# Kernel optimization log

Hardware: AMD Instinct MI355X
Metric: run time of the kernel (lower is better)

## Reference

```python
import jax, jax.numpy as jnp
import numpy as np

N = 50000      # nodes
E = 800000     # edges (avg degree 16)
IN = 128       # in_feats
HID = 32       # hidden_feats per head
H = 4          # num_heads
NEG_SLOPE = 0.2


def setup_inputs() -> dict:
    key = jax.random.key(0)
    ks = jax.random.split(key, 13)
    x = jax.random.normal(ks[0], (N, IN), jnp.float32)
    src = jax.random.randint(ks[1], (E,), 0, N, jnp.int32)
    dst = jax.random.randint(ks[2], (E,), 0, N, jnp.int32)

    def lin(k, fi, fo):
        return jax.random.normal(k, (fi, fo), jnp.float32) * (1.0 / np.sqrt(fi))

    # conv1: IN -> H*HID
    W1 = lin(ks[3], IN, H * HID)
    al1 = jax.random.normal(ks[4], (H, HID), jnp.float32) * 0.1
    ar1 = jax.random.normal(ks[5], (H, HID), jnp.float32) * 0.1
    b1 = jnp.zeros((H, HID), jnp.float32)
    # conv2: H*HID -> H*HID
    W2 = lin(ks[6], H * HID, H * HID)
    al2 = jax.random.normal(ks[7], (H, HID), jnp.float32) * 0.1
    ar2 = jax.random.normal(ks[8], (H, HID), jnp.float32) * 0.1
    b2 = jnp.zeros((H, HID), jnp.float32)
    # fc: HID -> 1
    fcW = lin(ks[9], HID, 1)
    fcb = jnp.zeros((1,), jnp.float32)
    return {"x": x, "src": src, "dst": dst,
            "W1": W1, "al1": al1, "ar1": ar1, "b1": b1,
            "W2": W2, "al2": al2, "ar2": ar2, "b2": b2,
            "fcW": fcW, "fcb": fcb}


def gat_conv(x, src, dst, W, al, ar, b):
    # x: [N, F_in] -> feat: [N, H, HID]
    feat = (x @ W).reshape(N, H, HID)
    el = jnp.sum(feat * al, axis=-1)            # [N, H]
    er = jnp.sum(feat * ar, axis=-1)            # [N, H]
    e = jax.nn.leaky_relu(el[src] + er[dst], NEG_SLOPE)  # [E, H]
    # segment softmax over incoming edges of each dst node
    m = jax.ops.segment_max(e, dst, num_segments=N)      # [N, H]
    ex = jnp.exp(e - m[dst])                              # [E, H]
    denom = jax.ops.segment_sum(ex, dst, num_segments=N)  # [N, H]
    alpha = ex / denom[dst]                                # [E, H]
    msg = feat[src] * alpha[:, :, None]                    # [E, H, HID]
    out = jax.ops.segment_sum(msg, dst, num_segments=N)   # [N, H, HID]
    return out + b[None, :, :]


def reference(x, src, dst, W1, al1, ar1, b1, W2, al2, ar2, b2, fcW, fcb):
    h = gat_conv(x, src, dst, W1, al1, ar1, b1).reshape(N, H * HID)
    h = jax.nn.relu(h)
    # dropout(0.5) is identity in eval mode
    h = gat_conv(h, src, dst, W2, al2, ar2, b2).mean(axis=1)  # [N, HID]
    return h @ fcW + fcb                                       # [N, 1]
```

## Files before the change

### kernel.cpp

```cpp
#include <hip/hip_runtime.h>
#include <hip/hip_fp16.h>

#define LEAK 0.2f
#define CAP 64

static __device__ inline unsigned pack_h2(float a, float b) {
    __half2 h = __floats2half2_rn(a, b);
    unsigned u; __builtin_memcpy(&u, &h, 4); return u;
}
static __device__ inline float2 unpack_h2(unsigned u) {
    __half2 h; __builtin_memcpy(&h, &u, 4); return __half22float2(h);
}

__global__ __launch_bounds__(256) void k0(
    int* __restrict__ cnt, const float* __restrict__ W2,
    const float* __restrict__ al2, const float* __restrict__ ar2,
    const float* __restrict__ fcW, const float* __restrict__ b2,
    float* __restrict__ WfT, float* __restrict__ bc, int N, int zb) {
    const int t = threadIdx.x;
    int i = blockIdx.x * 256 + t;
    if (i < N) cnt[i] = 0;
    int fb = blockIdx.x - zb;
    if (fb >= 0) {
        int idx = fb * 256 + t;
        if (idx < 1536) {
            int c = idx >> 7, k = idx & 127;
            int h = c & 3, sel = c >> 2;
            const float* vec = (sel == 0) ? (al2 + 32 * h)
                             : (sel == 1) ? (ar2 + 32 * h) : fcW;
            float s = 0.f;
#pragma unroll 8
            for (int m = 0; m < 32; m++) s += W2[k * 128 + 32 * h + m] * vec[m];
            WfT[c * 128 + k] = s;
        } else if (idx < 1540) {
            int h = idx - 1536;
            float s = 0.f;
            for (int m = 0; m < 32; m++) s += b2[h * 32 + m] * fcW[m];
            bc[h] = s;
        }
    }
}

__global__ __launch_bounds__(256, 4) void k1(
    const float* __restrict__ X, const float* __restrict__ W,
    const float* __restrict__ al, const float* __restrict__ ar,
    float* __restrict__ elh, float* __restrict__ erh,
    uint2* __restrict__ fh2,
    const int* __restrict__ src, const int* __restrict__ dst,
    int* __restrict__ cnt, unsigned short* __restrict__ ell,
    int N, int E, int ntiles, int nranks) {
    __shared__ float sW[32 * 128];
    __shared__ float sXT[32 * 128];
    const int b = blockIdx.x;
    const int t = threadIdx.x;

    if (b < ntiles) {
        const int r0 = b * 128;
        const int tx = t & 15;
        const int ty = t >> 4;
        const float4* X4 = (const float4*)X;
        const float4* W4 = (const float4*)W;
        float4* sW4 = (float4*)sW;
        const float4* sXT4 = (const float4*)sXT;

        float4 acc[8][2];
#pragma unroll
        for (int r = 0; r < 8; r++) {
            acc[r][0] = make_float4(0.f, 0.f, 0.f, 0.f);
            acc[r][1] = make_float4(0.f, 0.f, 0.f, 0.f);
        }
        for (int ks = 0; ks < 4; ++ks) {
            if (ks) __syncthreads();
#pragma unroll
            for (int i = 0; i < 4; i++) {
                int idx = i * 256 + t;
                sW4[idx] = W4[1024 * ks + idx];
            }
#pragma unroll
            for (int i = 0; i < 4; i++) {
                int idx = i * 256 + t;
                int row = idx >> 3;
                int kq = idx & 7;
                float4 v = make_float4(0.f, 0.f, 0.f, 0.f);
                if (r0 + row < N) v = X4[(size_t)(r0 + row) * 32 + ks * 8 + kq];
                int sc = (((row >> 2) ^ kq)) * 4 + (row & 3);
                sXT[(4 * kq + 0) * 128 + sc] = v.x;
                sXT[(4 * kq + 1) * 128 + sc] = v.y;
                sXT[(4 * kq + 2) * 128 + sc] = v.z;
                sXT[(4 * kq + 3) * 128 + sc] = v.w;
            }
            __syncthreads();
#pragma unroll 4
            for (int k = 0; k < 32; k++) {
                float4 w0 = sW4[k * 32 + tx];
                float4 w1 = sW4[k * 32 + 16 + tx];
                float4 x0 = sXT4[k * 32 + (ty ^ (k >> 2))];
                float4 x1 = sXT4[k * 32 + ((16 + ty) ^ (k >> 2))];
                float xs[8] = {x0.x, x0.y, x0.z, x0.w, x1.x, x1.y, x1.z, x1.w};
#pragma unroll
                for (int r = 0; r < 8; r++) {
                    acc[r][0].x += xs[r] * w0.x; acc[r][0].y += xs[r] * w0.y;
                    acc[r][0].z += xs[r] * w0.z; acc[r][0].w += xs[r] * w0.w;
                    acc[r][1].x += xs[r] * w1.x; acc[r][1].y += xs[r] * w1.y;
                    acc[r][1].z += xs[r] * w1.z; acc[r][1].w += xs[r] * w1.w;
                }
            }
        }
        const float4* al4p = (const float4*)al;
        const float4* ar4p = (const float4*)ar;
        float4 alA = al4p[tx], alB = al4p[16 + tx];
        float4 arA = ar4p[tx], arB = ar4p[16 + tx];
        const int hA = tx >> 3;
        const int hB = 2 + (tx >> 3);
        const int pA = tx & 7;
#pragma unroll
        for (int r = 0; r < 8; r++) {
            int lrow = (r < 4) ? (ty * 4 + r) : (64 + ty * 4 + (r - 4));
            int row = r0 + lrow;
            bool ok = row < N;
            float4 a0 = acc[r][0], a1 = acc[r][1];
            if (ok) {
                uint2 d0, d1;
                d0.x = pack_h2(a0.x, a0.y); d0.y = pack_h2(a0.z, a0.w);
                d1.x = pack_h2(a1.x, a1.y); d1.y = pack_h2(a1.z, a1.w);
                fh2[((size_t)hA * N + row) * 8 + pA] = d0;
                fh2[((size_t)hB * N + row) * 8 + pA] = d1;
            }
            float elA = a0.x * alA.x + a0.y * alA.y + a0.z * alA.z + a0.w * alA.w;
            float erA = a0.x * arA.x + a0.y * arA.y + a0.z * arA.z + a0.w * arA.w;
            float elB = a1.x * alB.x + a1.y * alB.y + a1.z * alB.z + a1.w * alB.w;
            float erB = a1.x * arB.x + a1.y * arB.y + a1.z * arB.z + a1.w * arB.w;
#pragma unroll
            for (int off = 1; off < 8; off <<= 1) {
                elA += __shfl_xor(elA, off); erA += __shfl_xor(erA, off);
                elB += __shfl_xor(elB, off); erB += __shfl_xor(erB, off);
            }
            if (ok && tx == 0) {
                elh[(size_t)0 * N + row] = elA; erh[(size_t)0 * N + row] = erA;
                elh[(size_t)2 * N + row] = elB; erh[(size_t)2 * N + row] = erB;
            }
            if (ok && tx == 8) {
                elh[(size_t)1 * N + row] = elA; erh[(size_t)1 * N + row] = erA;
                elh[(size_t)3 * N + row] = elB; erh[(size_t)3 * N + row] = erB;
            }
        }
    } else {
        const int bE = b - ntiles;
        const int part = bE & 7;
        const int rank = bE >> 3;
        const int S = (N + 7) >> 3;
        const int lo = part * S;
        const int hi = (lo + S < N) ? (lo + S) : N;
        const int per = (E + nranks - 1) / nranks;
        const int e0 = rank * per;
        const int e1 = (e0 + per < E) ? (e0 + per) : E;
        for (int e = e0 + t; e < e1; e += 256) {
            int d = dst[e];
            if (d >= lo && d < hi) {
                int s = src[e];
                int pos = atomicAdd(&cnt[d], 1);
                if (pos < CAP) ell[(size_t)d * CAP + pos] = (unsigned short)s;
            }
        }
    }
}

__global__ __launch_bounds__(256) void k_agg1(
    const uint2* __restrict__ fh2, const float* __restrict__ elh,
    const float* __restrict__ erh, const unsigned short* __restrict__ ell,
    const int* __restrict__ cnt, const float* __restrict__ b1,
    uint2* __restrict__ h1h2, int N, int ngrp) {
    const int wave = threadIdx.x >> 6;
    const int lane = threadIdx.x & 63;
    const int b = blockIdx.x;
    const int h = (b & 7) >> 1;
    const int g = (b >> 3) * 2 + (b & 1);
    if (g >= ngrp) return;
    const int nsub = lane >> 3;
    const int p = lane & 7;
    const int n = g * 32 + wave * 8 + nsub;
    const bool nok = n < N;

    int deg = 0;
    float er = 0.f;
    if (nok) {
        deg = cnt[n]; if (deg > CAP) deg = CAP;
        er = erh[(size_t)h * N + n];
    }
    const float* elp = elh + (size_t)h * N;
    const uint2* fhp = fh2 + (size_t)h * N * 8;
    const unsigned short* row = ell + (size_t)(nok ? n : 0) * CAP;

    float a0 = 0.f, a1 = 0.f, a2 = 0.f, a3 = 0.f, den = 0.f;
    int j = 0;
    for (; j + 3 < deg; j += 4) {
        ushort4 ss = *(const ushort4*)(row + j);
        int s0 = ss.x, s1 = ss.y, s2 = ss.z, s3 = ss.w;
        float e0 = elp[s0] + er;
        float e1 = elp[s1] + er;
        float e2 = elp[s2] + er;
        float e3 = elp[s3] + er;
        uint2 u0 = fhp[(size_t)s0 * 8 + p];
        uint2 u1 = fhp[(size_t)s1 * 8 + p];
        uint2 u2 = fhp[(size_t)s2 * 8 + p];
        uint2 u3 = fhp[(size_t)s3 * 8 + p];
        e0 = fmaxf(e0, LEAK * e0); float w0 = __expf(e0);
        e1 = fmaxf(e1, LEAK * e1); float w1 = __expf(e1);
        e2 = fmaxf(e2, LEAK * e2); float w2 = __expf(e2);
        e3 = fmaxf(e3, LEAK * e3); float w3 = __expf(e3);
        float2 f00 = unpack_h2(u0.x), f01 = unpack_h2(u0.y);
        float2 f10 = unpack_h2(u1.x), f11 = unpack_h2(u1.y);
        float2 f20 = unpack_h2(u2.x), f21 = unpack_h2(u2.y);
        float2 f30 = unpack_h2(u3.x), f31 = unpack_h2(u3.y);
        a0 += w0 * f00.x + w1 * f10.x + w2 * f20.x + w3 * f30.x;
        a1 += w0 * f00.y + w1 * f10.y + w2 * f20.y + w3 * f30.y;
        a2 += w0 * f01.x + w1 * f11.x + w2 * f21.x + w3 * f31.x;
        a3 += w0 * f01.y + w1 * f11.y + w2 * f21.y + w3 * f31.y;
        den += (w0 + w1) + (w2 + w3);
    }
    for (; j < deg; ++j) {
        int s = row[j];
        float e = elp[s] + er;
        uint2 u = fhp[(size_t)s * 8 + p];
        e = fmaxf(e, LEAK * e); float w = __expf(e);
        float2 f0 = unpack_h2(u.x), f1 = unpack_h2(u.y);
        a0 += w * f0.x; a1 += w * f0.y; a2 += w * f1.x; a3 += w * f1.y;
        den += w;
    }
    float inv = (den > 0.f) ? (1.0f / den) : 0.f;
    float4 bb = ((const float4*)b1)[h * 8 + p];
    a0 = fmaxf(a0 * inv + bb.x, 0.f);
    a1 = fmaxf(a1 * inv + bb.y, 0.f);
    a2 = fmaxf(a2 * inv + bb.z, 0.f);
    a3 = fmaxf(a3 * inv + bb.w, 0.f);
    if (nok) {
        uint2 d; d.x = pack_h2(a0, a1); d.y = pack_h2(a2, a3);
        h1h2[(size_t)n * 32 + h * 8 + p] = d;
    }
}

__global__ __launch_bounds__(256) void k_P(const uint2* __restrict__ h1h2,
                                           const float* __restrict__ WfT_g,
                                           float2* __restrict__ Pag,
                                           float* __restrict__ er2, int n_nodes) {
    __shared__ float sW[12 * 128];
    for (int i = threadIdx.x; i < 1536; i += 256) sW[i] = WfT_g[i];
    __syncthreads();
    int g = threadIdx.x >> 4;
    int q = threadIdx.x & 15;
    int n = blockIdx.x * 16 + g;
    if (n >= n_nodes) return;
    uint4 raw = ((const uint4*)h1h2)[(size_t)n * 16 + q];
    float2 f0 = unpack_h2(raw.x), f1 = unpack_h2(raw.y);
    float2 f2 = unpack_h2(raw.z), f3 = unpack_h2(raw.w);
    float hv[8] = {f0.x, f0.y, f1.x, f1.y, f2.x, f2.y, f3.x, f3.y};
    float p[12];
#pragma unroll
    for (int c = 0; c < 12; c++) {
        const float* wr = &sW[c * 128 + q * 8];
        float4 wa = *(const float4*)wr;
        float4 wb = *(const float4*)(wr + 4);
        p[c] = hv[0] * wa.x + hv[1] * wa.y + hv[2] * wa.z + hv[3] * wa.w
             + hv[4] * wb.x + hv[5] * wb.y + hv[6] * wb.z + hv[7] * wb.w;
    }
#pragma unroll
    for (int off = 1; off < 16; off <<= 1) {
#pragma unroll
        for (int c = 0; c < 12; c++) p[c] += __shfl_xor(p[c], off);
    }
    if (q < 4) Pag[(size_t)n * 4 + q] = make_float2(p[q], p[8 + q]);
    else if (q < 8) er2[(size_t)n * 4 + (q - 4)] = p[q];
}

__global__ __launch_bounds__(256) void k_agg2(const float2* __restrict__ Pag,
                                              const float* __restrict__ er2,
                                              const unsigned short* __restrict__ ell,
                                              const int* __restrict__ cnt,
                                              const float* __restrict__ bc,
                                              const float* __restrict__ fcb,
                                              float* __restrict__ out, int N) {
    int idx = blockIdx.x * 256 + threadIdx.x;
    int n = idx >> 2, h = idx & 3;
    if (n >= N) return;
    int deg = cnt[n]; if (deg > CAP) deg = CAP;
    float er = er2[(size_t)n * 4 + h];
    const unsigned short* row = ell + (size_t)n * CAP;
    float num = 0.f, den = 0.f;
    int j = 0, d4 = deg & ~3;
    for (; j < d4; j += 4) {
        ushort4 ss = *(const ushort4*)(row + j);
        int s0 = ss.x, s1 = ss.y, s2 = ss.z, s3 = ss.w;
        float2 g0 = Pag[(size_t)s0 * 4 + h];
        float2 g1 = Pag[(size_t)s1 * 4 + h];
        float2 g2 = Pag[(size_t)s2 * 4 + h];
        float2 g3 = Pag[(size_t)s3 * 4 + h];
        float e0 = g0.x + er; e0 = fmaxf(e0, LEAK * e0); float w0 = __expf(e0);
        float e1 = g1.x + er; e1 = fmaxf(e1, LEAK * e1); float w1 = __expf(e1);
        float e2 = g2.x + er; e2 = fmaxf(e2, LEAK * e2); float w2 = __expf(e2);
        float e3 = g3.x + er; e3 = fmaxf(e3, LEAK * e3); float w3 = __expf(e3);
        num += w0 * g0.y + w1 * g1.y + w2 * g2.y + w3 * g3.y;
        den += (w0 + w1) + (w2 + w3);
    }
    for (; j < deg; ++j) {
        int s = row[j];
        float2 gg = Pag[(size_t)s * 4 + h];
        float e = gg.x + er; e = fmaxf(e, LEAK * e);
        float w = __expf(e);
        num += w * gg.y; den += w;
    }
    float r = (den > 0.f) ? (num / den) : 0.f;
    r += bc[h];
    r += __shfl_xor(r, 1);
    r += __shfl_xor(r, 2);
    if (h == 0) out[n] = 0.25f * r + fcb[0];
}

extern "C" void kernel_launch(void* const* d_in, const int* in_sizes, int n_in,
                              void* d_out, int out_size, void* d_ws, size_t ws_size,
                              hipStream_t stream) {
    const float* x   = (const float*)d_in[0];
    const int* src   = (const int*)d_in[1];
    const int* dst   = (const int*)d_in[2];
    const float* W1  = (const float*)d_in[3];
    const float* al1 = (const float*)d_in[4];
    const float* ar1 = (const float*)d_in[5];
    const float* b1  = (const float*)d_in[6];
    const float* W2  = (const float*)d_in[7];
    const float* al2 = (const float*)d_in[8];
    const float* ar2 = (const float*)d_in[9];
    const float* b2  = (const float*)d_in[10];
    const float* fcW = (const float*)d_in[11];
    const float* fcb = (const float*)d_in[12];
    float* out = (float*)d_out;

    const int N = in_sizes[0] / 128;
    const int E = in_sizes[1];

    char* w = (char*)d_ws;
    size_t off = 0;
    auto alloc = [&](size_t bytes) {
        void* p = w + off;
        off = (off + bytes + 255) & ~(size_t)255;
        return p;
    };
    uint2* fh2   = (uint2*)alloc((size_t)4 * N * 8 * 8);
    uint2* h1h2  = (uint2*)alloc((size_t)N * 32 * 8);
    float* elh   = (float*)alloc((size_t)4 * N * 4);
    float* erhp  = (float*)alloc((size_t)4 * N * 4);
    float2* Pag  = (float2*)alloc((size_t)N * 4 * 8);
    float* er2   = (float*)alloc((size_t)N * 4 * 4);
    float* WfT   = (float*)alloc((size_t)(12 * 128 + 4) * 4);
    float* bc    = WfT + 12 * 128;
    int* cnt     = (int*)alloc((size_t)N * 4);
    unsigned short* ell = (unsigned short*)alloc((size_t)N * CAP * 2);

    const int zb = (N + 255) / 256;
    const int ntiles = (N + 127) / 128;
    const int nranks = 96;
    const int ellB = nranks * 8;
    const int ngrp = (N + 31) / 32;
    const int agg1_blocks = ((ngrp + 1) / 2) * 8;

    k0<<<zb + 8, 256, 0, stream>>>(cnt, W2, al2, ar2, fcW, b2, WfT, bc, N, zb);
    k1<<<ntiles + ellB, 256, 0, stream>>>(x, W1, al1, ar1, elh, erhp, fh2,
                                          src, dst, cnt, ell, N, E, ntiles, nranks);
    k_agg1<<<agg1_blocks, 256, 0, stream>>>(fh2, elh, erhp, ell, cnt, b1, h1h2, N, ngrp);
    k_P<<<(N + 15) / 16, 256, 0, stream>>>(h1h2, WfT, Pag, er2, N);
    k_agg2<<<(N * 4 + 255) / 256, 256, 0, stream>>>(Pag, er2, ell, cnt, bc, fcb, out, N);
}
```

Baseline: 229.8 us.

## Split ELL build from GEMM, node-major layouts, fuse layer-1 aggregation with projection

Moves ELL construction out of the GEMM kernel into its own simple edge-parallel kernel instead of partitioned ranks scanning all edges. Feature and attention-logit buffers switch from head-major to node-major layout, so one 16-lane group fetches a node's full 256-byte row across all heads in one gather. The layer-1 aggregation is fused with the k_P projection, which removes the h1 intermediate write and read and one launch. The costs are lane divergence from padding to the max degree within a wave, and an extra kernel launch for the ELL build.

```diff
diff --git a/kernel.cpp b/kernel.cpp
--- a/kernel.cpp
+++ b/kernel.cpp
@@ -41,223 +41,184 @@
     }
 }
 
-__global__ __launch_bounds__(256, 4) void k1(
+__global__ __launch_bounds__(256) void k_ell(
+    const int* __restrict__ src, const int* __restrict__ dst,
+    int* __restrict__ cnt, unsigned short* __restrict__ ell, int E) {
+    const int base = blockIdx.x * 1024 + threadIdx.x;
+#pragma unroll
+    for (int i = 0; i < 4; i++) {
+        int e = base + i * 256;
+        if (e < E) {
+            int s = src[e];
+            int d = dst[e];
+            int pos = atomicAdd(&cnt[d], 1);
+            if (pos < CAP) ell[(size_t)d * CAP + pos] = (unsigned short)s;
+        }
+    }
+}
+
+__global__ __launch_bounds__(256, 4) void k_gemm(
     const float* __restrict__ X, const float* __restrict__ W,
     const float* __restrict__ al, const float* __restrict__ ar,
-    float* __restrict__ elh, float* __restrict__ erh,
-    uint2* __restrict__ fh2,
-    const int* __restrict__ src, const int* __restrict__ dst,
-    int* __restrict__ cnt, unsigned short* __restrict__ ell,
-    int N, int E, int ntiles, int nranks) {
+    float* __restrict__ el_nh, float* __restrict__ er_nh,
+    uint2* __restrict__ fh2, int N) {
     __shared__ float sW[32 * 128];
     __shared__ float sXT[32 * 128];
-    const int b = blockIdx.x;
     const int t = threadIdx.x;
-
-    if (b < ntiles) {
-        const int r0 = b * 128;
-        const int tx = t & 15;
-        const int ty = t >> 4;
-        const float4* X4 = (const float4*)X;
-        const float4* W4 = (const float4*)W;
-        float4* sW4 = (float4*)sW;
-        const float4* sXT4 = (const float4*)sXT;
-
-        float4 acc[8][2];
-#pragma unroll
-        for (int r = 0; r < 8; r++) {
-            acc[r][0] = make_float4(0.f, 0.f, 0.f, 0.f);
-            acc[r][1] = make_float4(0.f, 0.f, 0.f, 0.f);
-        }
-        for (int ks = 0; ks < 4; ++ks) {
-            if (ks) __syncthreads();
-#pragma unroll
-            for (int i = 0; i < 4; i++) {
-                int idx = i * 256 + t;
-                sW4[idx] = W4[1024 * ks + idx];
+    const int r0 = blockIdx.x * 128;
+    const int tx = t & 15;
+    const int ty = t >> 4;
+    const float4* X4 = (const float4*)X;
+    const float4* W4 = (const float4*)W;
+    float4* sW4 = (float4*)sW;
+    const float4* sXT4 = (const float4*)sXT;
+
+    float4 acc[8][2];
+#pragma unroll
+    for (int r = 0; r < 8; r++) {
+        acc[r][0] = make_float4(0.f, 0.f, 0.f, 0.f);
+        acc[r][1] = make_float4(0.f, 0.f, 0.f, 0.f);
+    }
+    for (int ks = 0; ks < 4; ++ks) {
+        if (ks) __syncthreads();
+#pragma unroll
+        for (int i = 0; i < 4; i++) {
+            int idx = i * 256 + t;
+            sW4[idx] = W4[1024 * ks + idx];
+        }
+#pragma unroll
+        for (int i = 0; i < 4; i++) {
+            int idx = i * 256 + t;
+            int row = idx >> 3;
+            int kq = idx & 7;
+            float4 v = make_float4(0.f, 0.f, 0.f, 0.f);
+            if (r0 + row < N) v = X4[(size_t)(r0 + row) * 32 + ks * 8 + kq];
+            int sc = (((row >> 2) ^ kq)) * 4 + (row & 3);
+            sXT[(4 * kq + 0) * 128 + sc] = v.x;
+            sXT[(4 * kq + 1) * 128 + sc] = v.y;
+            sXT[(4 * kq + 2) * 128 + sc] = v.z;
+            sXT[(4 * kq + 3) * 128 + sc] = v.w;
+        }
+        __syncthreads();
+#pragma unroll 4
+        for (int k = 0; k < 32; k++) {
+            float4 w0 = sW4[k * 32 + tx];
+            float4 w1 = sW4[k * 32 + 16 + tx];
+            float4 x0 = sXT4[k * 32 + (ty ^ (k >> 2))];
+            float4 x1 = sXT4[k * 32 + ((16 + ty) ^ (k >> 2))];
+            float xs[8] = {x0.x, x0.y, x0.z, x0.w, x1.x, x1.y, x1.z, x1.w};
+#pragma unroll
+            for (int r = 0; r < 8; r++) {
+                acc[r][0].x += xs[r] * w0.x; acc[r][0].y += xs[r] * w0.y;
+                acc[r][0].z += xs[r] * w0.z; acc[r][0].w += xs[r] * w0.w;
+                acc[r][1].x += xs[r] * w1.x; acc[r][1].y += xs[r] * w1.y;
+                acc[r][1].z += xs[r] * w1.z; acc[r][1].w += xs[r] * w1.w;
             }
-#pragma unroll
-            for (int i = 0; i < 4; i++) {
-                int idx = i * 256 + t;
-                int row = idx >> 3;
-                int kq = idx & 7;
-                float4 v = make_float4(0.f, 0.f, 0.f, 0.f);
-                if (r0 + row < N) v = X4[(size_t)(r0 + row) * 32 + ks * 8 + kq];
-                int sc = (((row >> 2) ^ kq)) * 4 + (row & 3);
-                sXT[(4 * kq + 0) * 128 + sc] = v.x;
-                sXT[(4 * kq + 1) * 128 + sc] = v.y;
-                sXT[(4 * kq + 2) * 128 + sc] = v.z;
-                sXT[(4 * kq + 3) * 128 + sc] = v.w;
+        }
+    }
+    const float4* al4p = (const float4*)al;
+    const float4* ar4p = (const float4*)ar;
+    float4 alA = al4p[tx], alB = al4p[16 + tx];
+    float4 arA = ar4p[tx], arB = ar4p[16 + tx];
+#pragma unroll
+    for (int r = 0; r < 8; r++) {
+        int lrow = (r < 4) ? (ty * 4 + r) : (64 + ty * 4 + (r - 4));
+        int row = r0 + lrow;
+        bool ok = row < N;
+        float4 a0 = acc[r][0], a1 = acc[r][1];
+        if (ok) {
+            uint2 d0, d1;
+            d0.x = pack_h2(a0.x, a0.y); d0.y = pack_h2(a0.z, a0.w);
+            d1.x = pack_h2(a1.x, a1.y); d1.y = pack_h2(a1.z, a1.w);
+            fh2[(size_t)row * 32 + tx] = d0;
+            fh2[(size_t)row * 32 + 16 + tx] = d1;
+        }
+        float elA = a0.x * alA.x + a0.y * alA.y + a0.z * alA.z + a0.w * alA.w;
+        float erA = a0.x * arA.x + a0.y * arA.y + a0.z * arA.z + a0.w * arA.w;
+        float elB = a1.x * alB.x + a1.y * alB.y + a1.z * alB.z + a1.w * alB.w;
+        float erB = a1.x * arB.x + a1.y * arB.y + a1.z * arB.z + a1.w * arB.w;
+#pragma unroll
+        for (int off = 1; off < 8; off <<= 1) {
+            elA += __shfl_xor(elA, off); erA += __shfl_xor(erA, off);
+            elB += __shfl_xor(elB, off); erB += __shfl_xor(erB, off);
+        }
+        if (ok && tx == 0) {
+            el_nh[row * 4 + 0] = elA; er_nh[row * 4 + 0] = erA;
+            el_nh[row * 4 + 2] = elB; er_nh[row * 4 + 2] = erB;
+        }
+        if (ok && tx == 8) {
+            el_nh[row * 4 + 1] = elA; er_nh[row * 4 + 1] = erA;
+            el_nh[row * 4 + 3] = elB; er_nh[row * 4 + 3] = erB;
+        }
+    }
+}
+
+__global__ __launch_bounds__(256) void k_agg1P(
+    const uint2* __restrict__ fh2, const float* __restrict__ el_nh,
+    const float* __restrict__ er_nh, const unsigned short* __restrict__ ell,
+    const int* __restrict__ cnt, const float* __restrict__ b1,
+    const float* __restrict__ WfT, float2* __restrict__ Pag,
+    float* __restrict__ er2, int N) {
+    __shared__ float sWf[12 * 128];
+    for (int i = threadIdx.x; i < 1536; i += 256) sWf[i] = WfT[i];
+    __syncthreads();
+    const int wave = threadIdx.x >> 6, lane = threadIdx.x & 63;
+    const int nsub = lane >> 4, q = lane & 15, h = q >> 2;
+    const int g = blockIdx.x * 4 + wave;
+    const int n = g * 4 + nsub;
+    const bool nok = n < N;
+    const int nc = nok ? n : (N - 1);
+    int deg = nok ? cnt[n] : 0; if (deg > CAP) deg = CAP;
+    float er = nok ? er_nh[n * 4 + h] : 0.f;
+    const unsigned short* row = ell + (size_t)nc * CAP;
+    const uint4* fh4 = (const uint4*)fh2;
+
+    int dm = deg;
+    dm = max(dm, __shfl_xor(dm, 16));
+    dm = max(dm, __shfl_xor(dm, 32));
+
+    float acc[8] = {0.f, 0.f, 0.f, 0.f, 0.f, 0.f, 0.f, 0.f};
+    float den = 0.f;
+    for (int jt = 0; jt < dm; jt += 16) {
+        int s_all = (jt + q < CAP) ? (int)row[jt + q] : 0;
+        int lim = dm - jt; if (lim > 16) lim = 16;
+        for (int u = 0; u < lim; u += 4) {
+#pragma unroll
+            for (int v = 0; v < 4; v++) {
+                int jj = jt + u + v;
+                bool valid = jj < deg;
+                int s = __shfl(s_all, (lane & 48) | ((u + v) & 15));
+                s = valid ? s : 0;
+                float e = el_nh[s * 4 + h] + er;
+                e = fmaxf(e, LEAK * e);
+                float w = valid ? __expf(e) : 0.f;
+                uint4 f = fh4[(size_t)s * 16 + q];
+                float2 f0 = unpack_h2(f.x), f1 = unpack_h2(f.y);
+                float2 f2 = unpack_h2(f.z), f3 = unpack_h2(f.w);
+                acc[0] += w * f0.x; acc[1] += w * f0.y;
+                acc[2] += w * f1.x; acc[3] += w * f1.y;
+                acc[4] += w * f2.x; acc[5] += w * f2.y;
+                acc[6] += w * f3.x; acc[7] += w * f3.y;
+                den += w;
             }
-            __syncthreads();
-#pragma unroll 4
-            for (int k = 0; k < 32; k++) {
-                float4 w0 = sW4[k * 32 + tx];
-                float4 w1 = sW4[k * 32 + 16 + tx];
-                float4 x0 = sXT4[k * 32 + (ty ^ (k >> 2))];
-                float4 x1 = sXT4[k * 32 + ((16 + ty) ^ (k >> 2))];
-                float xs[8] = {x0.x, x0.y, x0.z, x0.w, x1.x, x1.y, x1.z, x1.w};
-#pragma unroll
-                for (int r = 0; r < 8; r++) {
-                    acc[r][0].x += xs[r] * w0.x; acc[r][0].y += xs[r] * w0.y;
-                    acc[r][0].z += xs[r] * w0.z; acc[r][0].w += xs[r] * w0.w;
-                    acc[r][1].x += xs[r] * w1.x; acc[r][1].y += xs[r] * w1.y;
-                    acc[r][1].z += xs[r] * w1.z; acc[r][1].w += xs[r] * w1.w;
-                }
-            }
-        }
-        const float4* al4p = (const float4*)al;
-        const float4* ar4p = (const float4*)ar;
-        float4 alA = al4p[tx], alB = al4p[16 + tx];
-        float4 arA = ar4p[tx], arB = ar4p[16 + tx];
-        const int hA = tx >> 3;
-        const int hB = 2 + (tx >> 3);
-        const int pA = tx & 7;
-#pragma unroll
-        for (int r = 0; r < 8; r++) {
-            int lrow = (r < 4) ? (ty * 4 + r) : (64 + ty * 4 + (r - 4));
-            int row = r0 + lrow;
-            bool ok = row < N;
-            float4 a0 = acc[r][0], a1 = acc[r][1];
-            if (ok) {
-                uint2 d0, d1;
-                d0.x = pack_h2(a0.x, a0.y); d0.y = pack_h2(a0.z, a0.w);
-                d1.x = pack_h2(a1.x, a1.y); d1.y = pack_h2(a1.z, a1.w);
-                fh2[((size_t)hA * N + row) * 8 + pA] = d0;
-                fh2[((size_t)hB * N + row) * 8 + pA] = d1;
-            }
-            float elA = a0.x * alA.x + a0.y * alA.y + a0.z * alA.z + a0.w * alA.w;
-            float erA = a0.x * arA.x + a0.y * arA.y + a0.z * arA.z + a0.w * arA.w;
-            float elB = a1.x * alB.x + a1.y * alB.y + a1.z * alB.z + a1.w * alB.w;
-            float erB = a1.x * arB.x + a1.y * arB.y + a1.z * arB.z + a1.w * arB.w;
-#pragma unroll
-            for (int off = 1; off < 8; off <<= 1) {
-                elA += __shfl_xor(elA, off); erA += __shfl_xor(erA, off);
-                elB += __shfl_xor(elB, off); erB += __shfl_xor(erB, off);
-            }
-            if (ok && tx == 0) {
-                elh[(size_t)0 * N + row] = elA; erh[(size_t)0 * N + row] = erA;
-                elh[(size_t)2 * N + row] = elB; erh[(size_t)2 * N + row] = erB;
-            }
-            if (ok && tx == 8) {
-                elh[(size_t)1 * N + row] = elA; erh[(size_t)1 * N + row] = erA;
-                elh[(size_t)3 * N + row] = elB; erh[(size_t)3 * N + row] = erB;
-            }
-        }
-    } else {
-        const int bE = b - ntiles;
-        const int part = bE & 7;
-        const int rank = bE >> 3;
-        const int S = (N + 7) >> 3;
-        const int lo = part * S;
-        const int hi = (lo + S < N) ? (lo + S) : N;
-        const int per = (E + nranks - 1) / nranks;
-        const int e0 = rank * per;
-        const int e1 = (e0 + per < E) ? (e0 + per) : E;
-        for (int e = e0 + t; e < e1; e += 256) {
-            int d = dst[e];
-            if (d >= lo && d < hi) {
-                int s = src[e];
-                int pos = atomicAdd(&cnt[d], 1);
-                if (pos < CAP) ell[(size_t)d * CAP + pos] = (unsigned short)s;
-            }
-        }
-    }
-}
-
-__global__ __launch_bounds__(256) void k_agg1(
-    const uint2* __restrict__ fh2, const float* __restrict__ elh,
-    const float* __restrict__ erh, const unsigned short* __restrict__ ell,
-    const int* __restrict__ cnt, const float* __restrict__ b1,
-    uint2* __restrict__ h1h2, int N, int ngrp) {
-    const int wave = threadIdx.x >> 6;
-    const int lane = threadIdx.x & 63;
-    const int b = blockIdx.x;
-    const int h = (b & 7) >> 1;
-    const int g = (b >> 3) * 2 + (b & 1);
-    if (g >= ngrp) return;
-    const int nsub = lane >> 3;
-    const int p = lane & 7;
-    const int n = g * 32 + wave * 8 + nsub;
-    const bool nok = n < N;
-
-    int deg = 0;
-    float er = 0.f;
-    if (nok) {
-        deg = cnt[n]; if (deg > CAP) deg = CAP;
-        er = erh[(size_t)h * N + n];
-    }
-    const float* elp = elh + (size_t)h * N;
-    const uint2* fhp = fh2 + (size_t)h * N * 8;
-    const unsigned short* row = ell + (size_t)(nok ? n : 0) * CAP;
-
-    float a0 = 0.f, a1 = 0.f, a2 = 0.f, a3 = 0.f, den = 0.f;
-    int j = 0;
-    for (; j + 3 < deg; j += 4) {
-        ushort4 ss = *(const ushort4*)(row + j);
-        int s0 = ss.x, s1 = ss.y, s2 = ss.z, s3 = ss.w;
-        float e0 = elp[s0] + er;
-        float e1 = elp[s1] + er;
-        float e2 = elp[s2] + er;
-        float e3 = elp[s3] + er;
-        uint2 u0 = fhp[(size_t)s0 * 8 + p];
-        uint2 u1 = fhp[(size_t)s1 * 8 + p];
-        uint2 u2 = fhp[(size_t)s2 * 8 + p];
-        uint2 u3 = fhp[(size_t)s3 * 8 + p];
-        e0 = fmaxf(e0, LEAK * e0); float w0 = __expf(e0);
-        e1 = fmaxf(e1, LEAK * e1); float w1 = __expf(e1);
-        e2 = fmaxf(e2, LEAK * e2); float w2 = __expf(e2);
-        e3 = fmaxf(e3, LEAK * e3); float w3 = __expf(e3);
-        float2 f00 = unpack_h2(u0.x), f01 = unpack_h2(u0.y);
-        float2 f10 = unpack_h2(u1.x), f11 = unpack_h2(u1.y);
-        float2 f20 = unpack_h2(u2.x), f21 = unpack_h2(u2.y);
-        float2 f30 = unpack_h2(u3.x), f31 = unpack_h2(u3.y);
-        a0 += w0 * f00.x + w1 * f10.x + w2 * f20.x + w3 * f30.x;
-        a1 += w0 * f00.y + w1 * f10.y + w2 * f20.y + w3 * f30.y;
-        a2 += w0 * f01.x + w1 * f11.x + w2 * f21.x + w3 * f31.x;
-        a3 += w0 * f01.y + w1 * f11.y + w2 * f21.y + w3 * f31.y;
-        den += (w0 + w1) + (w2 + w3);
-    }
-    for (; j < deg; ++j) {
-        int s = row[j];
-        float e = elp[s] + er;
-        uint2 u = fhp[(size_t)s * 8 + p];
-        e = fmaxf(e, LEAK * e); float w = __expf(e);
-        float2 f0 = unpack_h2(u.x), f1 = unpack_h2(u.y);
-        a0 += w * f0.x; a1 += w * f0.y; a2 += w * f1.x; a3 += w * f1.y;
-        den += w;
-    }
-    float inv = (den > 0.f) ? (1.0f / den) : 0.f;
-    float4 bb = ((const float4*)b1)[h * 8 + p];
-    a0 = fmaxf(a0 * inv + bb.x, 0.f);
-    a1 = fmaxf(a1 * inv + bb.y, 0.f);
-    a2 = fmaxf(a2 * inv + bb.z, 0.f);
-    a3 = fmaxf(a3 * inv + bb.w, 0.f);
-    if (nok) {
-        uint2 d; d.x = pack_h2(a0, a1); d.y = pack_h2(a2, a3);
-        h1h2[(size_t)n * 32 + h * 8 + p] = d;
-    }
-}
-
-__global__ __launch_bounds__(256) void k_P(const uint2* __restrict__ h1h2,
-                                           const float* __restrict__ WfT_g,
-                                           float2* __restrict__ Pag,
-                                           float* __restrict__ er2, int n_nodes) {
-    __shared__ float sW[12 * 128];
-    for (int i = threadIdx.x; i < 1536; i += 256) sW[i] = WfT_g[i];
-    __syncthreads();
-    int g = threadIdx.x >> 4;
-    int q = threadIdx.x & 15;
-    int n = blockIdx.x * 16 + g;
-    if (n >= n_nodes) return;
-    uint4 raw = ((const uint4*)h1h2)[(size_t)n * 16 + q];
-    float2 f0 = unpack_h2(raw.x), f1 = unpack_h2(raw.y);
-    float2 f2 = unpack_h2(raw.z), f3 = unpack_h2(raw.w);
-    float hv[8] = {f0.x, f0.y, f1.x, f1.y, f2.x, f2.y, f3.x, f3.y};
+        }
+    }
+    float inv = (den > 0.f) ? (1.f / den) : 0.f;
+    float4 b1a = ((const float4*)b1)[q * 2];
+    float4 b1b = ((const float4*)b1)[q * 2 + 1];
+    float hv[8];
+    hv[0] = fmaxf(acc[0] * inv + b1a.x, 0.f);
+    hv[1] = fmaxf(acc[1] * inv + b1a.y, 0.f);
+    hv[2] = fmaxf(acc[2] * inv + b1a.z, 0.f);
+    hv[3] = fmaxf(acc[3] * inv + b1a.w, 0.f);
+    hv[4] = fmaxf(acc[4] * inv + b1b.x, 0.f);
+    hv[5] = fmaxf(acc[5] * inv + b1b.y, 0.f);
+    hv[6] = fmaxf(acc[6] * inv + b1b.z, 0.f);
+    hv[7] = fmaxf(acc[7] * inv + b1b.w, 0.f);
     float p[12];
 #pragma unroll
     for (int c = 0; c < 12; c++) {
-        const float* wr = &sW[c * 128 + q * 8];
+        const float* wr = sWf + c * 128 + q * 8;
         float4 wa = *(const float4*)wr;
         float4 wb = *(const float4*)(wr + 4);
         p[c] = hv[0] * wa.x + hv[1] * wa.y + hv[2] * wa.z + hv[3] * wa.w
@@ -268,8 +229,10 @@
 #pragma unroll
         for (int c = 0; c < 12; c++) p[c] += __shfl_xor(p[c], off);
     }
-    if (q < 4) Pag[(size_t)n * 4 + q] = make_float2(p[q], p[8 + q]);
-    else if (q < 8) er2[(size_t)n * 4 + (q - 4)] = p[q];
+    if (nok) {
+        if (q < 4) Pag[(size_t)n * 4 + q] = make_float2(p[q], p[8 + q]);
+        else if (q < 8) er2[(size_t)n * 4 + (q - 4)] = p[q];
+    }
 }
 
 __global__ __launch_bounds__(256) void k_agg2(const float2* __restrict__ Pag,
@@ -343,10 +306,9 @@
         off = (off + bytes + 255) & ~(size_t)255;
         return p;
     };
-    uint2* fh2   = (uint2*)alloc((size_t)4 * N * 8 * 8);
-    uint2* h1h2  = (uint2*)alloc((size_t)N * 32 * 8);
-    float* elh   = (float*)alloc((size_t)4 * N * 4);
-    float* erhp  = (float*)alloc((size_t)4 * N * 4);
+    uint2* fh2   = (uint2*)alloc((size_t)N * 32 * 8);
+    float* el_nh = (float*)alloc((size_t)N * 4 * 4);
+    float* er_nh = (float*)alloc((size_t)N * 4 * 4);
     float2* Pag  = (float2*)alloc((size_t)N * 4 * 8);
     float* er2   = (float*)alloc((size_t)N * 4 * 4);
     float* WfT   = (float*)alloc((size_t)(12 * 128 + 4) * 4);
@@ -356,15 +318,13 @@
 
     const int zb = (N + 255) / 256;
     const int ntiles = (N + 127) / 128;
-    const int nranks = 96;
-    const int ellB = nranks * 8;
-    const int ngrp = (N + 31) / 32;
-    const int agg1_blocks = ((ngrp + 1) / 2) * 8;
+    const int ellB = (E + 1023) / 1024;
+    const int aggB = (N + 15) / 16;
 
     k0<<<zb + 8, 256, 0, stream>>>(cnt, W2, al2, ar2, fcW, b2, WfT, bc, N, zb);
-    k1<<<ntiles + ellB, 256, 0, stream>>>(x, W1, al1, ar1, elh, erhp, fh2,
-                                          src, dst, cnt, ell, N, E, ntiles, nranks);
-    k_agg1<<<agg1_blocks, 256, 0, stream>>>(fh2, elh, erhp, ell, cnt, b1, h1h2, N, ngrp);
-    k_P<<<(N + 15) / 16, 256, 0, stream>>>(h1h2, WfT, Pag, er2, N);
+    k_ell<<<ellB, 256, 0, stream>>>(src, dst, cnt, ell, E);
+    k_gemm<<<ntiles, 256, 0, stream>>>(x, W1, al1, ar1, el_nh, er_nh, fh2, N);
+    k_agg1P<<<aggB, 256, 0, stream>>>(fh2, el_nh, er_nh, ell, cnt, b1, WfT,
+                                      Pag, er2, N);
     k_agg2<<<(N * 4 + 255) / 256, 256, 0, stream>>>(Pag, er2, ell, cnt, bc, fcb, out, N);
 }
```

Result: no change. 230.8 us (+0.5%).
